# Kernel optimization log

Measured on AMD Instinct MI355X. Metric: run time of the kernel, lower is better.

## Reference

```python
import jax, jax.numpy as jnp
import numpy as np

R_MAX = 32
S_MAX = 2
C_Z = 128
IN_DIM = 4 * R_MAX + 2 * S_MAX + 7  # 139
N = 1024


def setup_inputs() -> dict:
    key = jax.random.key(0)
    k1, k2, k3, k4, k5, k6 = jax.random.split(key, 6)
    return {
        "asym_id": jax.random.randint(k1, (N,), 0, 8, dtype=jnp.int64 if jax.config.jax_enable_x64 else jnp.int32),
        "residue_index": jax.random.randint(k2, (N,), 0, 512),
        "entity_id": jax.random.randint(k3, (N,), 0, 4),
        "token_index": jax.random.randint(k4, (N,), 0, 2048),
        "sym_id": jax.random.randint(k5, (N,), 0, 4),
        "weight": jax.random.normal(k6, (C_Z, IN_DIM), dtype=jnp.float32),
    }


def reference(asym_id, residue_index, entity_id, token_index, sym_id, weight):
    r_max, s_max = R_MAX, S_MAX
    pos_dim = 2 * r_max + 2    # 66
    token_dim = 2 * r_max + 2  # 66
    # Pre-projected one-hot rows -> lookup tables (original casts to fp16, accumulates fp32)
    w16 = weight.astype(jnp.float16)
    W_pos = w16[:, :pos_dim].T                                # [66, c_z]
    W_token = w16[:, pos_dim:pos_dim + token_dim].T            # [66, c_z]
    W_entity = w16[:, pos_dim + token_dim]                     # [c_z]
    W_chain = w16[:, pos_dim + token_dim + 1:].T               # [6, c_z]

    same_chain = asym_id[:, None] == asym_id[None, :]          # [N, N]
    same_res = residue_index[:, None] == residue_index[None, :]
    same_ent = entity_id[:, None] == entity_id[None, :]

    d_res = jnp.clip(residue_index[:, None] - residue_index[None, :] + r_max, 0, 2 * r_max)
    d_res = jnp.where(same_chain, d_res, 2 * r_max + 1)

    d_tok = jnp.clip(token_index[:, None] - token_index[None, :] + r_max, 0, 2 * r_max)
    d_tok = jnp.where(same_chain & same_res, d_tok, 2 * r_max + 1)

    d_ch = jnp.clip(sym_id[:, None] - sym_id[None, :] + s_max, 0, 2 * s_max)
    d_ch = jnp.where(same_ent, d_ch, 2 * s_max + 1)

    out = (
        W_pos[d_res].astype(jnp.float32)
        + W_token[d_tok].astype(jnp.float32)
        + W_chain[d_ch].astype(jnp.float32)
        + jnp.where(same_ent[:, :, None], W_entity.astype(jnp.float32)[None, None, :], 0.0)
    )  # [N, N, c_z] fp32
    return out
```

## Files before the change

kernel.cpp:

```cpp
#include <hip/hip_runtime.h>
#include <hip/hip_fp16.h>

constexpr int NN    = 1024;
constexpr int CZ    = 128;
constexpr int INDIM = 139;

typedef float f4 __attribute__((ext_vector_type(4)));

constexpr int TBL_FLOATS = 18432;
constexpr int TBL_BYTES  = TBL_FLOATS * 4;

__global__ void build_tables(const int* __restrict__ asym, const int* __restrict__ resi,
                             const int* __restrict__ ent,  const int* __restrict__ tok,
                             const int* __restrict__ sym,  const float* __restrict__ w,
                             float* __restrict__ tbl, unsigned* __restrict__ packed)
{
    const int gtid   = blockIdx.x * 256 + threadIdx.x;
    const int stride = gridDim.x * 256;

    for (int idx = gtid; idx < 8448; idx += stride) {
        const int d = idx >> 7, c = idx & 127;
        tbl[idx]        = __half2float(__float2half(w[c * INDIM + d]));
        tbl[8448 + idx] = __half2float(__float2half(w[c * INDIM + 66 + d]));
    }
    for (int idx = gtid; idx < 768; idx += stride) {
        const int d = idx >> 7, c = idx & 127;
        const float ch = __half2float(__float2half(w[c * INDIM + 133 + d]));
        const float en = __half2float(__float2half(w[c * INDIM + 132]));
        tbl[16896 + idx]       = ch;
        tbl[16896 + 768 + idx] = ch + en;
    }
    for (int j = gtid; j < NN; j += stride) {
        packed[j] = (unsigned)(asym[j] & 7)
                  | ((unsigned)(ent[j]  & 3)    << 3)
                  | ((unsigned)(sym[j]  & 3)    << 5)
                  | ((unsigned)(resi[j] & 1023) << 7)
                  | ((unsigned)(tok[j]  & 4095) << 17);
    }
}

__global__ __launch_bounds__(256, 2) void relpos_main(
    const float* __restrict__ tbl, const unsigned* __restrict__ packed,
    float* __restrict__ out)
{
    __shared__ __attribute__((aligned(16))) float    lds[TBL_FLOATS];
    __shared__ __attribute__((aligned(16))) unsigned attrs[512];

    const int tid = threadIdx.x;

    {
        const f4* __restrict__ src = (const f4*)tbl;
        f4* __restrict__ dst = (f4*)lds;
        #pragma unroll
        for (int k = 0; k < 18; ++k) dst[tid + 256 * k] = src[tid + 256 * k];
    }

    const int bid   = blockIdx.x;
    const int i     = bid >> 1;
    const int jbase = (bid & 1) << 9;

    for (int k = tid; k < 512; k += 256) attrs[k] = packed[jbase + k];
    __syncthreads();

    const unsigned pi = packed[i];
    const int ai = pi & 7, ei = (pi >> 3) & 3, si = (pi >> 5) & 3;
    const int ri = (pi >> 7) & 1023, ti = (pi >> 17) & 4095;

    const int g  = tid >> 5;
    const int c4 = (tid & 31) << 2;

    float* outp = out + ((size_t)i << 17) + (size_t)(jbase + g) * CZ + c4;

    #pragma unroll 4
    for (int jt = 0; jt < 64; ++jt) {
        const unsigned pj = attrs[jt * 8 + g];
        const int aj = pj & 7, ej = (pj >> 3) & 3, sj = (pj >> 5) & 3;
        const int rj = (pj >> 7) & 1023, tj = (pj >> 17) & 4095;

        const bool sc = (ai == aj);
        const bool sr = (ri == rj);
        const int  se = (ei == ej) ? 1 : 0;

        int dres = min(max(ri - rj + 32, 0), 64);
        if (!sc) dres = 65;
        int dtok = min(max(ti - tj + 32, 0), 64);
        if (!(sc && sr)) dtok = 65;
        int dch = min(max(si - sj + 2, 0), 4);
        if (!se) dch = 5;

        const f4 p  = *(const f4*)&lds[dres * 128 + c4];
        const f4 t  = *(const f4*)&lds[8448 + dtok * 128 + c4];
        const f4 cc = *(const f4*)&lds[16896 + se * 768 + dch * 128 + c4];

        __builtin_nontemporal_store(p + t + cc, (f4*)outp);
        outp += 8 * CZ;
    }
}

extern "C" void kernel_launch(void* const* d_in, const int* in_sizes, int n_in,
                              void* d_out, int out_size, void* d_ws, size_t ws_size,
                              hipStream_t stream) {
    const int*   asym   = (const int*)d_in[0];
    const int*   resi   = (const int*)d_in[1];
    const int*   ent    = (const int*)d_in[2];
    const int*   tok    = (const int*)d_in[3];
    const int*   sym    = (const int*)d_in[4];
    const float* weight = (const float*)d_in[5];
    float*       out    = (float*)d_out;

    float*    tbl    = (float*)d_ws;
    unsigned* packed = (unsigned*)((char*)d_ws + TBL_BYTES);

    build_tables<<<16, 256, 0, stream>>>(asym, resi, ent, tok, sym, weight, tbl, packed);
    relpos_main<<<NN * 2, 256, 0, stream>>>(tbl, packed, out);
}
```

Baseline: 530.7 us.

## Store lookup tables as fp16 in LDS and process a full row per block

Lookup tables move from fp32 to fp16 in LDS and are converted on the fly, with the entity term added as a float vector multiplied by a mask. This roughly halves LDS usage so launch bounds can rise to four blocks per CU. Each block now covers a full output row of 1024 columns, which halves the number of blocks and the per-block table loads. Output stores change from nontemporal to regular stores, which may alter cache behaviour on the 512MB write stream.

```diff
diff --git a/kernel.cpp b/kernel.cpp
--- a/kernel.cpp
+++ b/kernel.cpp
@@ -7,29 +7,40 @@
 
 typedef float f4 __attribute__((ext_vector_type(4)));
 
-constexpr int TBL_FLOATS = 18432;
-constexpr int TBL_BYTES  = TBL_FLOATS * 4;
+constexpr int H_TOTAL  = 17664;
+constexpr int H_BYTES  = H_TOTAL * 2;
+constexpr int H_F4     = H_BYTES / 16;
+
+
+struct __attribute__((aligned(8))) h4 { __half a, b, c, d; };
+
+__device__ __forceinline__ f4 h4_to_f4(h4 h) {
+    f4 r;
+    r.x = __half2float(h.a); r.y = __half2float(h.b);
+    r.z = __half2float(h.c); r.w = __half2float(h.d);
+    return r;
+}
 
 __global__ void build_tables(const int* __restrict__ asym, const int* __restrict__ resi,
                              const int* __restrict__ ent,  const int* __restrict__ tok,
                              const int* __restrict__ sym,  const float* __restrict__ w,
-                             float* __restrict__ tbl, unsigned* __restrict__ packed)
+                             __half* __restrict__ htbl, float* __restrict__ entf,
+                             unsigned* __restrict__ packed)
 {
     const int gtid   = blockIdx.x * 256 + threadIdx.x;
     const int stride = gridDim.x * 256;
 
     for (int idx = gtid; idx < 8448; idx += stride) {
         const int d = idx >> 7, c = idx & 127;
-        tbl[idx]        = __half2float(__float2half(w[c * INDIM + d]));
-        tbl[8448 + idx] = __half2float(__float2half(w[c * INDIM + 66 + d]));
+        htbl[idx]        = __float2half(w[c * INDIM + d]);
+        htbl[8448 + idx] = __float2half(w[c * INDIM + 66 + d]);
     }
     for (int idx = gtid; idx < 768; idx += stride) {
         const int d = idx >> 7, c = idx & 127;
-        const float ch = __half2float(__float2half(w[c * INDIM + 133 + d]));
-        const float en = __half2float(__float2half(w[c * INDIM + 132]));
-        tbl[16896 + idx]       = ch;
-        tbl[16896 + 768 + idx] = ch + en;
+        htbl[16896 + idx] = __float2half(w[c * INDIM + 133 + d]);
     }
+    for (int c = gtid; c < CZ; c += stride)
+        entf[c] = __half2float(__float2half(w[c * INDIM + 132]));
     for (int j = gtid; j < NN; j += stride) {
         packed[j] = (unsigned)(asym[j] & 7)
                   | ((unsigned)(ent[j]  & 3)    << 3)
@@ -39,60 +50,67 @@
     }
 }
 
-__global__ __launch_bounds__(256, 2) void relpos_main(
-    const float* __restrict__ tbl, const unsigned* __restrict__ packed,
-    float* __restrict__ out)
+__global__ __launch_bounds__(256, 4) void relpos_main(
+    const __half* __restrict__ htbl, const float* __restrict__ entf,
+    const unsigned* __restrict__ packed, float* __restrict__ out)
 {
-    __shared__ __attribute__((aligned(16))) float    lds[TBL_FLOATS];
-    __shared__ __attribute__((aligned(16))) unsigned attrs[512];
+    __shared__ __attribute__((aligned(16))) __half   hl[H_TOTAL];
+    __shared__ __attribute__((aligned(16))) unsigned attrs[NN];
 
     const int tid = threadIdx.x;
 
     {
-        const f4* __restrict__ src = (const f4*)tbl;
-        f4* __restrict__ dst = (f4*)lds;
+        const f4* __restrict__ src = (const f4*)htbl;
+        f4* __restrict__ dst = (f4*)hl;
         #pragma unroll
-        for (int k = 0; k < 18; ++k) dst[tid + 256 * k] = src[tid + 256 * k];
+        for (int k = 0; k < 9; ++k) {
+            const int idx = tid + 256 * k;
+            if (idx < H_F4) dst[idx] = src[idx];
+        }
     }
-
-    const int bid   = blockIdx.x;
-    const int i     = bid >> 1;
-    const int jbase = (bid & 1) << 9;
-
-    for (int k = tid; k < 512; k += 256) attrs[k] = packed[jbase + k];
-    __syncthreads();
-
-    const unsigned pi = packed[i];
-    const int ai = pi & 7, ei = (pi >> 3) & 3, si = (pi >> 5) & 3;
-    const int ri = (pi >> 7) & 1023, ti = (pi >> 17) & 4095;
+    #pragma unroll
+    for (int k = 0; k < 4; ++k) attrs[tid + 256 * k] = packed[tid + 256 * k];
 
     const int g  = tid >> 5;
     const int c4 = (tid & 31) << 2;
+    const f4 ev = *(const f4*)&entf[c4];
 
-    float* outp = out + ((size_t)i << 17) + (size_t)(jbase + g) * CZ + c4;
+    __syncthreads();
+
+    const int i = blockIdx.x;
+    const unsigned pi = attrs[i];
+    const int a0 = pi & 7, e0 = (pi >> 3) & 3, s0 = (pi >> 5) & 3;
+    const int r0 = (pi >> 7) & 1023, t0 = (pi >> 17) & 4095;
+
+    float* outp = out + ((size_t)i << 17) + (size_t)g * CZ + c4;
 
     #pragma unroll 4
-    for (int jt = 0; jt < 64; ++jt) {
+    for (int jt = 0; jt < 128; ++jt) {
         const unsigned pj = attrs[jt * 8 + g];
         const int aj = pj & 7, ej = (pj >> 3) & 3, sj = (pj >> 5) & 3;
         const int rj = (pj >> 7) & 1023, tj = (pj >> 17) & 4095;
 
-        const bool sc = (ai == aj);
-        const bool sr = (ri == rj);
-        const int  se = (ei == ej) ? 1 : 0;
+        const bool sc  = (a0 == aj);
+        const bool sr  = (r0 == rj);
+        const bool seb = (e0 == ej);
 
-        int dres = min(max(ri - rj + 32, 0), 64);
+        int dres = min(max(r0 - rj + 32, 0), 64);
         if (!sc) dres = 65;
-        int dtok = min(max(ti - tj + 32, 0), 64);
+        int dtok = min(max(t0 - tj + 32, 0), 64);
         if (!(sc && sr)) dtok = 65;
-        int dch = min(max(si - sj + 2, 0), 4);
-        if (!se) dch = 5;
+        int dch = min(max(s0 - sj + 2, 0), 4);
+        if (!seb) dch = 5;
+        const float sef = seb ? 1.0f : 0.0f;
 
-        const f4 p  = *(const f4*)&lds[dres * 128 + c4];
-        const f4 t  = *(const f4*)&lds[8448 + dtok * 128 + c4];
-        const f4 cc = *(const f4*)&lds[16896 + se * 768 + dch * 128 + c4];
+        const h4 ph = *(const h4*)&hl[dres * 128 + c4];
+        const h4 th = *(const h4*)&hl[8448 + dtok * 128 + c4];
+        const h4 ch = *(const h4*)&hl[16896 + dch * 128 + c4];
 
-        __builtin_nontemporal_store(p + t + cc, (f4*)outp);
+        f4 o = h4_to_f4(ph) + h4_to_f4(th);
+        o = o + h4_to_f4(ch);
+        o = o + sef * ev;
+
+        *(f4*)outp = o;
         outp += 8 * CZ;
     }
 }
@@ -108,9 +126,11 @@
     const float* weight = (const float*)d_in[5];
     float*       out    = (float*)d_out;
 
-    float*    tbl    = (float*)d_ws;
-    unsigned* packed = (unsigned*)((char*)d_ws + TBL_BYTES);
+    __half*   htbl   = (__half*)d_ws;
+    float*    entf   = (float*)((char*)d_ws + H_BYTES);
+    unsigned* packed = (unsigned*)((char*)d_ws + H_BYTES + 512);
 
-    build_tables<<<16, 256, 0, stream>>>(asym, resi, ent, tok, sym, weight, tbl, packed);
-    relpos_main<<<NN * 2, 256, 0, stream>>>(tbl, packed, out);
+    build_tables<<<16, 256, 0, stream>>>(asym, resi, ent, tok, sym, weight,
+                                         htbl, entf, packed);
+    relpos_main<<<NN, 256, 0, stream>>>(htbl, entf, packed, out);
 }
```

Measured after the change: 540.8 us. Within noise of the previous version (+1.9%).
